# Performance work log

Measured on AMD Instinct MI355X. Metric: run time of the kernel, lower is better.

## Reference

```python
import jax, jax.numpy as jnp
import numpy as np

G = 4096        # graphs
NPG = 32        # nodes per graph
N = G * NPG     # total nodes
D = 256         # hidden (inv node feat) dim
SH = 256        # shared / node-MLP hidden dim
HDG = 50        # graph head dim
HDN = 3         # node head dim
NB = 2          # num branches (dataset IDs)


def setup_inputs() -> dict:
    key = jax.random.key(0)
    ks = jax.random.split(key, 8)
    s = 0.02
    return {
        "x": jax.random.normal(ks[0], (N, D), jnp.float32),
        "dataset_name": jax.random.randint(ks[1], (G,), 0, NB, jnp.int32),
        "batch": (jnp.arange(N) // NPG).astype(jnp.int32),
        "Wgs": jax.random.normal(ks[2], (NB, D, SH), jnp.float32) * s,
        "bgs": jnp.zeros((NB, SH), jnp.float32),
        "Wgh": jax.random.normal(ks[3], (NB, SH, 2 * HDG), jnp.float32) * s,
        "bgh": jnp.zeros((NB, 2 * HDG), jnp.float32),
        "Wn1": jax.random.normal(ks[4], (NB, D, SH), jnp.float32) * s,
        "bn1": jnp.zeros((NB, SH), jnp.float32),
        "Wn2": jax.random.normal(ks[5], (NB, SH, 2 * HDN), jnp.float32) * s,
        "bn2": jnp.zeros((NB, 2 * HDN), jnp.float32),
    }


def reference(x, dataset_name, batch, Wgs, bgs, Wgh, bgh, Wn1, bn1, Wn2, bn2):
    n_nodes = x.shape[0]
    n_graphs = dataset_name.shape[0]

    # ---- graph pooling (mean) : scatter-reduce nodes -> graphs ----
    counts = jax.ops.segment_sum(jnp.ones((n_nodes,), x.dtype), batch, num_segments=n_graphs)
    x_graph = jax.ops.segment_sum(x, batch, num_segments=n_graphs) / counts[:, None]  # [G, D]

    # ---- graph head: per-branch shared MLP + head, then branch dispatch ----
    hg = jax.nn.relu(jnp.einsum("gd,bds->bgs", x_graph, Wgs) + bgs[:, None, :])       # [B, G, SH]
    og = jnp.einsum("bgs,bsh->bgh", hg, Wgh) + bgh[:, None, :]                        # [B, G, 2*HDG]
    out_g = og[dataset_name, jnp.arange(n_graphs)]                                    # [G, 2*HDG]
    g_head = out_g[:, :HDG]
    g_var = out_g[:, HDG:] ** 2

    # ---- node head (mlp type): per-branch MLP on nodes, dispatch by node's graph ID ----
    node_branch = dataset_name[batch]                                                 # [N]
    hn = jax.nn.relu(jnp.einsum("nd,bds->bns", x, Wn1) + bn1[:, None, :])             # [B, N, SH]
    on = jnp.einsum("bns,bsh->bnh", hn, Wn2) + bn2[:, None, :]                        # [B, N, 2*HDN]
    out_n = on[node_branch, jnp.arange(n_nodes)]                                      # [N, 2*HDN]
    n_head = out_n[:, :HDN]
    n_var = out_n[:, HDN:] ** 2

    # (outputs, outputs_var) flattened: heads then variance heads
    return (g_head, n_head, g_var, n_var)
```

## Files before the change

### kernel.cpp

```cpp
#include <hip/hip_runtime.h>
#include <hip/hip_bf16.h>


#define G_   4096
#define NPG_ 32
#define NN_  (G_*NPG_)
#define D_   256
#define SH_  256
#define HDG_ 50
#define HDN_ 3

#define OFF_GH 0
#define OFF_NH (G_*HDG_)
#define OFF_GV (OFF_NH + NN_*HDN_)
#define OFF_NV (OFF_GV + G_*HDG_)

typedef short v8s __attribute__((ext_vector_type(8)));
typedef short v4s __attribute__((ext_vector_type(4)));
typedef float v4f __attribute__((ext_vector_type(4)));

__device__ __forceinline__ float bfu2f(unsigned short u) {
    return __uint_as_float(((unsigned int)u) << 16);
}
__device__ __forceinline__ unsigned short f2bfu(float v) {
    __hip_bfloat16 b = __float2bfloat16(v);
    return *reinterpret_cast<unsigned short*>(&b);
}

#define MFMA16(a, b, c) __builtin_amdgcn_mfma_f32_16x16x32_bf16((a), (b), (c), 0, 0, 0)

__global__ __launch_bounds__(256) void prep(const float* __restrict__ Wn1,
                                            const float* __restrict__ Wgs,
                                            const float* __restrict__ Wgh,
                                            const float* __restrict__ Wn2,
                                            unsigned short* __restrict__ wout,
                                            const int* __restrict__ dsname,
                                            int* __restrict__ glist,
                                            int* __restrict__ gcnt) {
    const int blk = blockIdx.x;
    const int t = threadIdx.x;
    if (blk < 1312) {
        const int idx = blk * 256 + t;
        float v;
        if (idx < 131072) {
            const int b = idx >> 16, rem = idx & 65535, s = rem >> 8, d = rem & 255;
            v = Wn1[b * 65536 + d * 256 + s];
        } else if (idx < 262144) {
            const int i2 = idx - 131072;
            const int np = i2 >> 8, d = i2 & 255;
            v = Wgs[(np >> 8) * 65536 + d * 256 + (np & 255)];
        } else if (idx < 327680) {
            const int i3 = idx - 262144;
            const int npp = i3 >> 8, k = i3 & 255;
            const int b = npp >> 7, c = npp & 127;
            v = (c < 100) ? Wgh[b * 25600 + k * 100 + c] : 0.f;
        } else {
            const int i4 = idx - 327680;
            const int b = i4 >> 12, rem = i4 & 4095, n = rem >> 8, k = rem & 255;
            v = (n < 6) ? Wn2[b * 1536 + k * 6 + n] : 0.f;
        }
        wout[idx] = f2bfu(v);
    } else {
        __shared__ int cnt[2];
        if (t < 2) cnt[t] = 0;
        __syncthreads();
        for (int i = 0; i < 16; i++) {
            const int g = i * 256 + t;
            const int b = dsname[g];
            const int slot = atomicAdd(&cnt[b], 1);
            glist[b * G_ + slot] = g;
        }
        __syncthreads();
        if (t < 2) gcnt[t] = cnt[t];
    }
}

__global__ __launch_bounds__(512) void node_pers2(const float* __restrict__ x,
                                                  const int* __restrict__ glist,
                                                  const int* __restrict__ gcnt,
                                                  const unsigned short* __restrict__ Wn1T,
                                                  const float* __restrict__ bn1,
                                                  const unsigned short* __restrict__ Wn2b,
                                                  const float* __restrict__ bn2,
                                                  unsigned short* __restrict__ xg,
                                                  float* __restrict__ out) {
    __shared__ __align__(16) unsigned short xs[64 * 264];
    __shared__ __align__(16) unsigned short hs[64 * 264];
    __shared__ __align__(16) float red[16 * 256];
    const int t = threadIdx.x;
    const int wave = t >> 6, lane = t & 63;
    const int l15 = lane & 15, quad = lane >> 4;
    const int br = blockIdx.x & 1;
    const int bslot = blockIdx.x >> 1;
    const int cnt = gcnt[br];
    const int ntile = (cnt + 1) >> 1;

    const int base_n = (wave & 1) * 128 + (wave >> 1) * 32;

    v8s B1[2][8];
    float bias1[2];
    #pragma unroll
    for (int nt = 0; nt < 2; nt++) {
        const unsigned short* bp = Wn1T + br * 65536 + (base_n + nt * 16 + l15) * 256 + quad * 8;
        #pragma unroll
        for (int kt = 0; kt < 8; kt++) B1[nt][kt] = *(const v8s*)(bp + kt * 32);
        bias1[nt] = bn1[br * 256 + base_n + nt * 16 + l15];
    }

    v8s B2[8];
    {
        const unsigned short* bp = Wn2b + br * 4096 + l15 * 256 + quad * 8;
        #pragma unroll
        for (int kt = 0; kt < 8; kt++) B2[kt] = *(const v8s*)(bp + kt * 32);
    }
    float bias2 = 0.f;
    if (l15 < 6) bias2 = bn2[br * 6 + l15];

    const int r0 = t >> 6;
    const int colb = (t & 63) * 4;

    float4 pv[8];
    int ga = 0, gb = 0;
    if (bslot < ntile) {
        const int i0 = 2 * bslot, i1 = i0 + 1;
        ga = glist[br * G_ + i0];
        gb = glist[br * G_ + ((i1 < cnt) ? i1 : cnt - 1)];
        const float* xa = x + (size_t)ga * 8192 + r0 * 256 + colb;
        const float* xb = x + (size_t)gb * 8192 + r0 * 256 + colb;
        #pragma unroll
        for (int k = 0; k < 4; k++) {
            pv[k]     = *(const float4*)(xa + k * 2048);
            pv[4 + k] = *(const float4*)(xb + k * 2048);
        }
    }

    for (int ti = bslot; ti < ntile; ti += 128) {
        const int gA = ga, gB = gb;

        float4 sa = make_float4(0.f, 0.f, 0.f, 0.f);
        float4 sb = make_float4(0.f, 0.f, 0.f, 0.f);
        #pragma unroll
        for (int k = 0; k < 4; k++) {
            const float4 va = pv[k], vb = pv[4 + k];
            sa.x += va.x; sa.y += va.y; sa.z += va.z; sa.w += va.w;
            sb.x += vb.x; sb.y += vb.y; sb.z += vb.z; sb.w += vb.w;
            v4s bva, bvb;
            bva[0] = (short)f2bfu(va.x); bva[1] = (short)f2bfu(va.y);
            bva[2] = (short)f2bfu(va.z); bva[3] = (short)f2bfu(va.w);
            bvb[0] = (short)f2bfu(vb.x); bvb[1] = (short)f2bfu(vb.y);
            bvb[2] = (short)f2bfu(vb.z); bvb[3] = (short)f2bfu(vb.w);
            *(v4s*)(&xs[(r0 + 8 * k) * 264 + colb])      = bva;
            *(v4s*)(&xs[(32 + r0 + 8 * k) * 264 + colb]) = bvb;
        }
        *(float4*)(&red[r0 * 256 + colb])       = sa;
        *(float4*)(&red[(8 + r0) * 256 + colb]) = sb;

        {
            const int tn = ti + 128;
            if (tn < ntile) {
                const int i0 = 2 * tn, i1 = i0 + 1;
                ga = glist[br * G_ + i0];
                gb = glist[br * G_ + ((i1 < cnt) ? i1 : cnt - 1)];
                const float* xa = x + (size_t)ga * 8192 + r0 * 256 + colb;
                const float* xb = x + (size_t)gb * 8192 + r0 * 256 + colb;
                #pragma unroll
                for (int k = 0; k < 4; k++) {
                    pv[k]     = *(const float4*)(xa + k * 2048);
                    pv[4 + k] = *(const float4*)(xb + k * 2048);
                }
            }
        }
        __syncthreads();

        {
            const int g = t >> 8, c = t & 255;
            float m = 0.f;
            #pragma unroll
            for (int r = 0; r < 8; r++) m += red[(g * 8 + r) * 256 + c];
            xg[(size_t)(g ? gB : gA) * 256 + c] = f2bfu(m * (1.0f / NPG_));
        }

        v4f acc[4][2];
        #pragma unroll
        for (int mt = 0; mt < 4; mt++)
            #pragma unroll
            for (int nt = 0; nt < 2; nt++) acc[mt][nt] = (v4f){0.f, 0.f, 0.f, 0.f};
        #pragma unroll
        for (int kt = 0; kt < 8; kt++) {
            const int ko = kt * 32 + quad * 8;
            v8s a0 = *(const v8s*)(&xs[(     l15) * 264 + ko]);
            v8s a1 = *(const v8s*)(&xs[(16 + l15) * 264 + ko]);
            v8s a2 = *(const v8s*)(&xs[(32 + l15) * 264 + ko]);
            v8s a3 = *(const v8s*)(&xs[(48 + l15) * 264 + ko]);
            #pragma unroll
            for (int nt = 0; nt < 2; nt++) {
                acc[0][nt] = MFMA16(a0, B1[nt][kt], acc[0][nt]);
                acc[1][nt] = MFMA16(a1, B1[nt][kt], acc[1][nt]);
                acc[2][nt] = MFMA16(a2, B1[nt][kt], acc[2][nt]);
                acc[3][nt] = MFMA16(a3, B1[nt][kt], acc[3][nt]);
            }
        }

        #pragma unroll
        for (int nt = 0; nt < 2; nt++) {
            const int col = base_n + nt * 16 + l15;
            #pragma unroll
            for (int mt = 0; mt < 4; mt++)
                #pragma unroll
                for (int r = 0; r < 4; r++) {
                    const int row = mt * 16 + quad * 4 + r;
                    const float v = acc[mt][nt][r] + bias1[nt];
                    hs[row * 264 + col] = f2bfu(v > 0.f ? v : 0.f);
                }
        }
        __syncthreads();

        if (wave < 4) {
            v4f a2 = (v4f){0.f, 0.f, 0.f, 0.f};
            #pragma unroll
            for (int kt = 0; kt < 8; kt++) {
                v8s av = *(const v8s*)(&hs[(wave * 16 + l15) * 264 + kt * 32 + quad * 8]);
                a2 = MFMA16(av, B2[kt], a2);
            }
            if (l15 < 6) {
                #pragma unroll
                for (int r = 0; r < 4; r++) {
                    const int row = wave * 16 + quad * 4 + r;
                    const int g = (row < 32) ? gA : gB;
                    const int n = g * NPG_ + (row & 31);
                    const float v = a2[r] + bias2;
                    if (l15 < HDN_) out[OFF_NH + n * HDN_ + l15] = v;
                    else            out[OFF_NV + n * HDN_ + (l15 - HDN_)] = v * v;
                }
            }
        }
    }
}

__global__ __launch_bounds__(256) void graph_mfma2(const unsigned short* __restrict__ xg,
                                                   const int* __restrict__ dsname,
                                                   const unsigned short* __restrict__ WgsT,
                                                   const float* __restrict__ bgs,
                                                   const unsigned short* __restrict__ WghP,
                                                   const float* __restrict__ bgh,
                                                   float* __restrict__ out) {
    __shared__ __align__(16) unsigned short xs[32 * 264];
    __shared__ int bls[32];
    const int gbase = blockIdx.x * 32;
    const int t = threadIdx.x;
    const int wave = t >> 6, lane = t & 63;
    const int l15 = lane & 15, quad = lane >> 4;
    if (t < 32) bls[t] = dsname[gbase + t];

    #pragma unroll
    for (int k = 0; k < 4; k++) {
        const int flat = k * 2048 + t * 8;
        *(v8s*)(&xs[(flat >> 8) * 264 + (flat & 255)]) =
            *(const v8s*)(xg + (size_t)gbase * 256 + flat);
    }
    __syncthreads();

    v4f acc[2][8];
    #pragma unroll
    for (int mt = 0; mt < 2; mt++)
        #pragma unroll
        for (int nt = 0; nt < 8; nt++) acc[mt][nt] = (v4f){0.f, 0.f, 0.f, 0.f};

    const unsigned short* Ab = &xs[l15 * 264 + quad * 8];
    const unsigned short* Bb = WgsT + (wave * 128 + l15) * 256 + quad * 8;

    #pragma unroll
    for (int kt = 0; kt < 8; kt++) {
        const int ko = kt * 32;
        v8s a0 = *(const v8s*)(Ab + ko);
        v8s a1 = *(const v8s*)(Ab + 16 * 264 + ko);
        #pragma unroll
        for (int nt = 0; nt < 8; nt++) {
            v8s bv = *(const v8s*)(Bb + nt * 16 * 256 + ko);
            acc[0][nt] = MFMA16(a0, bv, acc[0][nt]);
            acc[1][nt] = MFMA16(a1, bv, acc[1][nt]);
        }
    }
    __syncthreads();

    {
        const int bw = wave >> 1;
        #pragma unroll
        for (int nt = 0; nt < 8; nt++) {
            const int sp = wave * 128 + nt * 16 + l15;
            const int s_local = sp & 255;
            const float bias = bgs[sp];
            #pragma unroll
            for (int mt = 0; mt < 2; mt++)
                #pragma unroll
                for (int r = 0; r < 4; r++) {
                    const int row = mt * 16 + quad * 4 + r;
                    if (bls[row] == bw) {
                        const float v = acc[mt][nt][r] + bias;
                        xs[row * 264 + s_local] = f2bfu(v > 0.f ? v : 0.f);
                    }
                }
        }
    }
    __syncthreads();

    v4f acc2[2][4];
    #pragma unroll
    for (int mt = 0; mt < 2; mt++)
        #pragma unroll
        for (int nt = 0; nt < 4; nt++) acc2[mt][nt] = (v4f){0.f, 0.f, 0.f, 0.f};

    const unsigned short* B2 = WghP + ((wave * 4) * 16 + l15) * 256 + quad * 8;
    #pragma unroll
    for (int kt = 0; kt < 8; kt++) {
        const int ko = kt * 32;
        v8s a0 = *(const v8s*)(&xs[l15 * 264 + ko + quad * 8]);
        v8s a1 = *(const v8s*)(&xs[(16 + l15) * 264 + ko + quad * 8]);
        #pragma unroll
        for (int nt = 0; nt < 4; nt++) {
            v8s bv = *(const v8s*)(B2 + nt * 16 * 256 + ko);
            acc2[0][nt] = MFMA16(a0, bv, acc2[0][nt]);
            acc2[1][nt] = MFMA16(a1, bv, acc2[1][nt]);
        }
    }

    #pragma unroll
    for (int nt = 0; nt < 4; nt++) {
        const int npp  = (wave * 4 + nt) * 16 + l15;
        const int bo   = npp >> 7, c = npp & 127;
        if (c < 2 * HDG_) {
            const float bias = bgh[bo * 2 * HDG_ + c];
            #pragma unroll
            for (int mt = 0; mt < 2; mt++)
                #pragma unroll
                for (int r = 0; r < 4; r++) {
                    const int row = mt * 16 + quad * 4 + r;
                    if (bls[row] == bo) {
                        const float o = acc2[mt][nt][r] + bias;
                        const int g = gbase + row;
                        if (c < HDG_) out[OFF_GH + g * HDG_ + c] = o;
                        else          out[OFF_GV + g * HDG_ + (c - HDG_)] = o * o;
                    }
                }
        }
    }
}

extern "C" void kernel_launch(void* const* d_in, const int* in_sizes, int n_in,
                              void* d_out, int out_size, void* d_ws, size_t ws_size,
                              hipStream_t stream) {
    const float* x      = (const float*)d_in[0];
    const int*   dsname = (const int*)d_in[1];
    const float* Wgs = (const float*)d_in[3];
    const float* bgs = (const float*)d_in[4];
    const float* Wgh = (const float*)d_in[5];
    const float* bgh = (const float*)d_in[6];
    const float* Wn1 = (const float*)d_in[7];
    const float* bn1 = (const float*)d_in[8];
    const float* Wn2 = (const float*)d_in[9];
    const float* bn2 = (const float*)d_in[10];
    float* out = (float*)d_out;

    unsigned short* wsbuf = (unsigned short*)d_ws;
    unsigned short* Wn1T  = wsbuf;
    unsigned short* WgsT  = wsbuf + 131072;
    unsigned short* WghP  = wsbuf + 262144;
    unsigned short* Wn2b  = wsbuf + 327680;
    unsigned short* xg    = wsbuf + 335872;
    int* glist = (int*)((char*)d_ws + 2768896);
    int* gcnt  = (int*)((char*)d_ws + 2801664);

    prep       <<<1313,    256, 0, stream>>>(Wn1, Wgs, Wgh, Wn2, wsbuf, dsname, glist, gcnt);
    node_pers2 <<<256,     512, 0, stream>>>(x, glist, gcnt, Wn1T, bn1, Wn2b, bn2, xg, out);
    graph_mfma2<<<G_ / 32, 256, 0, stream>>>(xg, dsname, WgsT, bgs, WghP, bgh, out);
}
```

Before: 246.8 us.

## Fold weight prep and graph bucketing into the persistent node kernel

Removes the separate prep kernel. Each node block now converts its slice of the graph-head weights to bf16, computes its own per-branch graph list through a block-wide prefix scan over dataset IDs, and loads the Wn1/Wn2 fragments straight from fp32 with a transpose and bf16 conversion done in registers. This drops one kernel launch and the global round trip for glist and the transposed node weights. In exchange every block rescans all dataset IDs and does strided, uncoalesced fp32 weight gathers.

```diff
diff --git a/kernel.cpp b/kernel.cpp
--- a/kernel.cpp
+++ b/kernel.cpp
@@ -19,9 +19,6 @@
 typedef short v4s __attribute__((ext_vector_type(4)));
 typedef float v4f __attribute__((ext_vector_type(4)));
 
-__device__ __forceinline__ float bfu2f(unsigned short u) {
-    return __uint_as_float(((unsigned int)u) << 16);
-}
 __device__ __forceinline__ unsigned short f2bfu(float v) {
     __hip_bfloat16 b = __float2bfloat16(v);
     return *reinterpret_cast<unsigned short*>(&b);
@@ -29,89 +26,115 @@
 
 #define MFMA16(a, b, c) __builtin_amdgcn_mfma_f32_16x16x32_bf16((a), (b), (c), 0, 0, 0)
 
-__global__ __launch_bounds__(256) void prep(const float* __restrict__ Wn1,
-                                            const float* __restrict__ Wgs,
-                                            const float* __restrict__ Wgh,
-                                            const float* __restrict__ Wn2,
-                                            unsigned short* __restrict__ wout,
-                                            const int* __restrict__ dsname,
-                                            int* __restrict__ glist,
-                                            int* __restrict__ gcnt) {
-    const int blk = blockIdx.x;
-    const int t = threadIdx.x;
-    if (blk < 1312) {
-        const int idx = blk * 256 + t;
-        float v;
-        if (idx < 131072) {
-            const int b = idx >> 16, rem = idx & 65535, s = rem >> 8, d = rem & 255;
-            v = Wn1[b * 65536 + d * 256 + s];
-        } else if (idx < 262144) {
-            const int i2 = idx - 131072;
-            const int np = i2 >> 8, d = i2 & 255;
-            v = Wgs[(np >> 8) * 65536 + d * 256 + (np & 255)];
-        } else if (idx < 327680) {
-            const int i3 = idx - 262144;
-            const int npp = i3 >> 8, k = i3 & 255;
-            const int b = npp >> 7, c = npp & 127;
-            v = (c < 100) ? Wgh[b * 25600 + k * 100 + c] : 0.f;
-        } else {
-            const int i4 = idx - 327680;
-            const int b = i4 >> 12, rem = i4 & 4095, n = rem >> 8, k = rem & 255;
-            v = (n < 6) ? Wn2[b * 1536 + k * 6 + n] : 0.f;
-        }
-        wout[idx] = f2bfu(v);
-    } else {
-        __shared__ int cnt[2];
-        if (t < 2) cnt[t] = 0;
-        __syncthreads();
-        for (int i = 0; i < 16; i++) {
-            const int g = i * 256 + t;
-            const int b = dsname[g];
-            const int slot = atomicAdd(&cnt[b], 1);
-            glist[b * G_ + slot] = g;
-        }
-        __syncthreads();
-        if (t < 2) gcnt[t] = cnt[t];
-    }
-}
-
-__global__ __launch_bounds__(512) void node_pers2(const float* __restrict__ x,
-                                                  const int* __restrict__ glist,
-                                                  const int* __restrict__ gcnt,
-                                                  const unsigned short* __restrict__ Wn1T,
-                                                  const float* __restrict__ bn1,
-                                                  const unsigned short* __restrict__ Wn2b,
-                                                  const float* __restrict__ bn2,
-                                                  unsigned short* __restrict__ xg,
-                                                  float* __restrict__ out) {
+__global__ __launch_bounds__(512) void node_all(const float* __restrict__ x,
+                                                const int* __restrict__ dsname,
+                                                const float* __restrict__ Wn1,
+                                                const float* __restrict__ bn1,
+                                                const float* __restrict__ Wn2,
+                                                const float* __restrict__ bn2,
+                                                const float* __restrict__ Wgs,
+                                                const float* __restrict__ Wgh,
+                                                unsigned short* __restrict__ WgsT,
+                                                unsigned short* __restrict__ WghP,
+                                                unsigned short* __restrict__ xg,
+                                                float* __restrict__ out) {
     __shared__ __align__(16) unsigned short xs[64 * 264];
     __shared__ __align__(16) unsigned short hs[64 * 264];
     __shared__ __align__(16) float red[16 * 256];
+    __shared__ int glds[32];
+    __shared__ int scanS[10];
     const int t = threadIdx.x;
     const int wave = t >> 6, lane = t & 63;
     const int l15 = lane & 15, quad = lane >> 4;
     const int br = blockIdx.x & 1;
     const int bslot = blockIdx.x >> 1;
-    const int cnt = gcnt[br];
+
+    {
+        const int e0 = blockIdx.x * 768;
+        #pragma unroll
+        for (int i = 0; i < 2; i++) {
+            const int ii = t + i * 512;
+            if (ii < 768) {
+                const int e = e0 + ii;
+                if (e < 131072) {
+                    const int np = e >> 8, d = e & 255;
+                    WgsT[e] = f2bfu(Wgs[(np >> 8) * 65536 + d * 256 + (np & 255)]);
+                } else {
+                    const int i3 = e - 131072;
+                    const int npp = i3 >> 8, k = i3 & 255;
+                    const int b = npp >> 7, c = npp & 127;
+                    WghP[i3] = f2bfu((c < 100) ? Wgh[b * 25600 + k * 100 + c] : 0.f);
+                }
+            }
+        }
+    }
+
+    int pre, c0;
+    {
+        c0 = 0;
+        #pragma unroll
+        for (int k = 0; k < 8; k++) c0 += (dsname[t * 8 + k] == br) ? 1 : 0;
+        pre = c0;
+        #pragma unroll
+        for (int d = 1; d < 64; d <<= 1) {
+            const int o = __shfl_up(pre, d);
+            if (lane >= d) pre += o;
+        }
+        if (lane == 63) scanS[wave] = pre;
+    }
+    __syncthreads();
+    if (t == 0) {
+        int s = 0;
+        #pragma unroll
+        for (int w = 0; w < 8; w++) { const int v = scanS[w]; scanS[w] = s; s += v; }
+        scanS[8] = s;
+    }
+    __syncthreads();
+    const int cnt = scanS[8];
     const int ntile = (cnt + 1) >> 1;
+    {
+        int slot = scanS[wave] + (pre - c0);
+        for (int k = 0; k < 8; k++) {
+            const int g = t * 8 + k;
+            if (dsname[g] == br) {
+                const int ti2 = slot >> 1;
+                const int q = ti2 - bslot;
+                if (q >= 0 && (q & 127) == 0 && (q >> 7) < 16)
+                    glds[(q >> 7) * 2 + (slot & 1)] = g;
+                if (slot == cnt - 1) scanS[9] = g;
+                slot++;
+            }
+        }
+    }
+    __syncthreads();
 
     const int base_n = (wave & 1) * 128 + (wave >> 1) * 32;
-
     v8s B1[2][8];
     float bias1[2];
     #pragma unroll
     for (int nt = 0; nt < 2; nt++) {
-        const unsigned short* bp = Wn1T + br * 65536 + (base_n + nt * 16 + l15) * 256 + quad * 8;
-        #pragma unroll
-        for (int kt = 0; kt < 8; kt++) B1[nt][kt] = *(const v8s*)(bp + kt * 32);
-        bias1[nt] = bn1[br * 256 + base_n + nt * 16 + l15];
-    }
-
+        const int s = base_n + nt * 16 + l15;
+        const float* wp = Wn1 + br * 65536 + s;
+        #pragma unroll
+        for (int kt = 0; kt < 8; kt++) {
+            v8s f;
+            #pragma unroll
+            for (int j = 0; j < 8; j++)
+                f[j] = (short)f2bfu(wp[(kt * 32 + quad * 8 + j) * 256]);
+            B1[nt][kt] = f;
+        }
+        bias1[nt] = bn1[br * 256 + s];
+    }
     v8s B2[8];
-    {
-        const unsigned short* bp = Wn2b + br * 4096 + l15 * 256 + quad * 8;
-        #pragma unroll
-        for (int kt = 0; kt < 8; kt++) B2[kt] = *(const v8s*)(bp + kt * 32);
+    #pragma unroll
+    for (int kt = 0; kt < 8; kt++) {
+        v8s f;
+        #pragma unroll
+        for (int j = 0; j < 8; j++) {
+            const int k = kt * 32 + quad * 8 + j;
+            f[j] = (l15 < 6) ? (short)f2bfu(Wn2[br * 1536 + k * 6 + l15]) : (short)0;
+        }
+        B2[kt] = f;
     }
     float bias2 = 0.f;
     if (l15 < 6) bias2 = bn2[br * 6 + l15];
@@ -122,9 +145,8 @@
     float4 pv[8];
     int ga = 0, gb = 0;
     if (bslot < ntile) {
-        const int i0 = 2 * bslot, i1 = i0 + 1;
-        ga = glist[br * G_ + i0];
-        gb = glist[br * G_ + ((i1 < cnt) ? i1 : cnt - 1)];
+        ga = glds[0];
+        gb = (2 * bslot + 1 < cnt) ? glds[1] : scanS[9];
         const float* xa = x + (size_t)ga * 8192 + r0 * 256 + colb;
         const float* xb = x + (size_t)gb * 8192 + r0 * 256 + colb;
         #pragma unroll
@@ -158,9 +180,9 @@
         {
             const int tn = ti + 128;
             if (tn < ntile) {
-                const int i0 = 2 * tn, i1 = i0 + 1;
-                ga = glist[br * G_ + i0];
-                gb = glist[br * G_ + ((i1 < cnt) ? i1 : cnt - 1)];
+                const int ix = (tn - bslot) >> 7;
+                ga = glds[ix * 2];
+                gb = (2 * tn + 1 < cnt) ? glds[ix * 2 + 1] : scanS[9];
                 const float* xa = x + (size_t)ga * 8192 + r0 * 256 + colb;
                 const float* xb = x + (size_t)gb * 8192 + r0 * 256 + colb;
                 #pragma unroll
@@ -362,15 +384,11 @@
     float* out = (float*)d_out;
 
     unsigned short* wsbuf = (unsigned short*)d_ws;
-    unsigned short* Wn1T  = wsbuf;
     unsigned short* WgsT  = wsbuf + 131072;
     unsigned short* WghP  = wsbuf + 262144;
-    unsigned short* Wn2b  = wsbuf + 327680;
     unsigned short* xg    = wsbuf + 335872;
-    int* glist = (int*)((char*)d_ws + 2768896);
-    int* gcnt  = (int*)((char*)d_ws + 2801664);
-
-    prep       <<<1313,    256, 0, stream>>>(Wn1, Wgs, Wgh, Wn2, wsbuf, dsname, glist, gcnt);
-    node_pers2 <<<256,     512, 0, stream>>>(x, glist, gcnt, Wn1T, bn1, Wn2b, bn2, xg, out);
+
+    node_all   <<<256,     512, 0, stream>>>(x, dsname, Wn1, bn1, Wn2, bn2,
+                                             Wgs, Wgh, WgsT, WghP, xg, out);
     graph_mfma2<<<G_ / 32, 256, 0, stream>>>(xg, dsname, WgsT, bgs, WghP, bgh, out);
 }
```

Result: no change. 248.9 us (+0.9%).

## Replace persistent node kernel with one-tile-per-block launch and shared LDS buffer

Applied to the files above, without the earlier changes.

The persistent 256-block node kernel, which looped over graph-pair tiles with register prefetch of the next tile, becomes a 4096-block grid where each block handles one graph pair and returns early if it has no work. The hidden-activation LDS buffer is removed and the x tile buffer is reused for it, with an extra barrier added before the overwrite. The smaller LDS footprint is meant to allow more resident blocks per CU, so the hardware scheduler hides load latency in place of the manual prefetch. In exchange, every block reloads the Wn1/Wn2 weight fragments into registers, and about half of the blocks launch only to exit immediately.

```diff
diff --git a/kernel.cpp b/kernel.cpp
--- a/kernel.cpp
+++ b/kernel.cpp
@@ -19,9 +19,6 @@
 typedef short v4s __attribute__((ext_vector_type(4)));
 typedef float v4f __attribute__((ext_vector_type(4)));
 
-__device__ __forceinline__ float bfu2f(unsigned short u) {
-    return __uint_as_float(((unsigned int)u) << 16);
-}
 __device__ __forceinline__ unsigned short f2bfu(float v) {
     __hip_bfloat16 b = __float2bfloat16(v);
     return *reinterpret_cast<unsigned short*>(&b);
@@ -75,25 +72,29 @@
     }
 }
 
-__global__ __launch_bounds__(512) void node_pers2(const float* __restrict__ x,
-                                                  const int* __restrict__ glist,
-                                                  const int* __restrict__ gcnt,
-                                                  const unsigned short* __restrict__ Wn1T,
-                                                  const float* __restrict__ bn1,
-                                                  const unsigned short* __restrict__ Wn2b,
-                                                  const float* __restrict__ bn2,
-                                                  unsigned short* __restrict__ xg,
-                                                  float* __restrict__ out) {
+__global__ __launch_bounds__(512) void node_tile(const float* __restrict__ x,
+                                                 const int* __restrict__ glist,
+                                                 const int* __restrict__ gcnt,
+                                                 const unsigned short* __restrict__ Wn1T,
+                                                 const float* __restrict__ bn1,
+                                                 const unsigned short* __restrict__ Wn2b,
+                                                 const float* __restrict__ bn2,
+                                                 unsigned short* __restrict__ xg,
+                                                 float* __restrict__ out) {
     __shared__ __align__(16) unsigned short xs[64 * 264];
-    __shared__ __align__(16) unsigned short hs[64 * 264];
     __shared__ __align__(16) float red[16 * 256];
     const int t = threadIdx.x;
     const int wave = t >> 6, lane = t & 63;
     const int l15 = lane & 15, quad = lane >> 4;
     const int br = blockIdx.x & 1;
     const int bslot = blockIdx.x >> 1;
+
     const int cnt = gcnt[br];
-    const int ntile = (cnt + 1) >> 1;
+    if (2 * bslot >= cnt) return;
+
+    const int gA = glist[br * G_ + 2 * bslot];
+    const int gB = (2 * bslot + 1 < cnt) ? glist[br * G_ + 2 * bslot + 1]
+                                         : glist[br * G_ + cnt - 1];
 
     const int base_n = (wave & 1) * 128 + (wave >> 1) * 32;
 
@@ -106,42 +107,26 @@
         for (int kt = 0; kt < 8; kt++) B1[nt][kt] = *(const v8s*)(bp + kt * 32);
         bias1[nt] = bn1[br * 256 + base_n + nt * 16 + l15];
     }
-
     v8s B2[8];
     {
         const unsigned short* bp = Wn2b + br * 4096 + l15 * 256 + quad * 8;
         #pragma unroll
         for (int kt = 0; kt < 8; kt++) B2[kt] = *(const v8s*)(bp + kt * 32);
     }
-    float bias2 = 0.f;
-    if (l15 < 6) bias2 = bn2[br * 6 + l15];
+    const float bias2 = (l15 < 6) ? bn2[br * 6 + l15] : 0.f;
 
     const int r0 = t >> 6;
     const int colb = (t & 63) * 4;
 
-    float4 pv[8];
-    int ga = 0, gb = 0;
-    if (bslot < ntile) {
-        const int i0 = 2 * bslot, i1 = i0 + 1;
-        ga = glist[br * G_ + i0];
-        gb = glist[br * G_ + ((i1 < cnt) ? i1 : cnt - 1)];
-        const float* xa = x + (size_t)ga * 8192 + r0 * 256 + colb;
-        const float* xb = x + (size_t)gb * 8192 + r0 * 256 + colb;
-        #pragma unroll
-        for (int k = 0; k < 4; k++) {
-            pv[k]     = *(const float4*)(xa + k * 2048);
-            pv[4 + k] = *(const float4*)(xb + k * 2048);
-        }
-    }
-
-    for (int ti = bslot; ti < ntile; ti += 128) {
-        const int gA = ga, gB = gb;
-
+    {
+        const float* xa = x + (size_t)gA * 8192 + r0 * 256 + colb;
+        const float* xb = x + (size_t)gB * 8192 + r0 * 256 + colb;
         float4 sa = make_float4(0.f, 0.f, 0.f, 0.f);
         float4 sb = make_float4(0.f, 0.f, 0.f, 0.f);
         #pragma unroll
         for (int k = 0; k < 4; k++) {
-            const float4 va = pv[k], vb = pv[4 + k];
+            const float4 va = *(const float4*)(xa + k * 2048);
+            const float4 vb = *(const float4*)(xb + k * 2048);
             sa.x += va.x; sa.y += va.y; sa.z += va.z; sa.w += va.w;
             sb.x += vb.x; sb.y += vb.y; sb.z += vb.z; sb.w += vb.w;
             v4s bva, bvb;
@@ -154,84 +139,69 @@
         }
         *(float4*)(&red[r0 * 256 + colb])       = sa;
         *(float4*)(&red[(8 + r0) * 256 + colb]) = sb;
-
-        {
-            const int tn = ti + 128;
-            if (tn < ntile) {
-                const int i0 = 2 * tn, i1 = i0 + 1;
-                ga = glist[br * G_ + i0];
-                gb = glist[br * G_ + ((i1 < cnt) ? i1 : cnt - 1)];
-                const float* xa = x + (size_t)ga * 8192 + r0 * 256 + colb;
-                const float* xb = x + (size_t)gb * 8192 + r0 * 256 + colb;
-                #pragma unroll
-                for (int k = 0; k < 4; k++) {
-                    pv[k]     = *(const float4*)(xa + k * 2048);
-                    pv[4 + k] = *(const float4*)(xb + k * 2048);
-                }
-            }
-        }
-        __syncthreads();
-
-        {
-            const int g = t >> 8, c = t & 255;
-            float m = 0.f;
-            #pragma unroll
-            for (int r = 0; r < 8; r++) m += red[(g * 8 + r) * 256 + c];
-            xg[(size_t)(g ? gB : gA) * 256 + c] = f2bfu(m * (1.0f / NPG_));
-        }
-
-        v4f acc[4][2];
+    }
+    __syncthreads();
+
+    {
+        const int g = t >> 8, c = t & 255;
+        float m = 0.f;
+        #pragma unroll
+        for (int r = 0; r < 8; r++) m += red[(g * 8 + r) * 256 + c];
+        xg[(size_t)(g ? gB : gA) * 256 + c] = f2bfu(m * (1.0f / NPG_));
+    }
+
+    v4f acc[4][2];
+    #pragma unroll
+    for (int mt = 0; mt < 4; mt++)
+        #pragma unroll
+        for (int nt = 0; nt < 2; nt++) acc[mt][nt] = (v4f){0.f, 0.f, 0.f, 0.f};
+    #pragma unroll
+    for (int kt = 0; kt < 8; kt++) {
+        const int ko = kt * 32 + quad * 8;
+        v8s a0 = *(const v8s*)(&xs[(     l15) * 264 + ko]);
+        v8s a1 = *(const v8s*)(&xs[(16 + l15) * 264 + ko]);
+        v8s a2 = *(const v8s*)(&xs[(32 + l15) * 264 + ko]);
+        v8s a3 = *(const v8s*)(&xs[(48 + l15) * 264 + ko]);
+        #pragma unroll
+        for (int nt = 0; nt < 2; nt++) {
+            acc[0][nt] = MFMA16(a0, B1[nt][kt], acc[0][nt]);
+            acc[1][nt] = MFMA16(a1, B1[nt][kt], acc[1][nt]);
+            acc[2][nt] = MFMA16(a2, B1[nt][kt], acc[2][nt]);
+            acc[3][nt] = MFMA16(a3, B1[nt][kt], acc[3][nt]);
+        }
+    }
+    __syncthreads();
+
+    #pragma unroll
+    for (int nt = 0; nt < 2; nt++) {
+        const int col = base_n + nt * 16 + l15;
         #pragma unroll
         for (int mt = 0; mt < 4; mt++)
             #pragma unroll
-            for (int nt = 0; nt < 2; nt++) acc[mt][nt] = (v4f){0.f, 0.f, 0.f, 0.f};
+            for (int r = 0; r < 4; r++) {
+                const int row = mt * 16 + quad * 4 + r;
+                const float v = acc[mt][nt][r] + bias1[nt];
+                xs[row * 264 + col] = f2bfu(v > 0.f ? v : 0.f);
+            }
+    }
+    __syncthreads();
+
+    if (wave < 4) {
+        v4f a2 = (v4f){0.f, 0.f, 0.f, 0.f};
         #pragma unroll
         for (int kt = 0; kt < 8; kt++) {
-            const int ko = kt * 32 + quad * 8;
-            v8s a0 = *(const v8s*)(&xs[(     l15) * 264 + ko]);
-            v8s a1 = *(const v8s*)(&xs[(16 + l15) * 264 + ko]);
-            v8s a2 = *(const v8s*)(&xs[(32 + l15) * 264 + ko]);
-            v8s a3 = *(const v8s*)(&xs[(48 + l15) * 264 + ko]);
+            v8s av = *(const v8s*)(&xs[(wave * 16 + l15) * 264 + kt * 32 + quad * 8]);
+            a2 = MFMA16(av, B2[kt], a2);
+        }
+        if (l15 < 6) {
             #pragma unroll
-            for (int nt = 0; nt < 2; nt++) {
-                acc[0][nt] = MFMA16(a0, B1[nt][kt], acc[0][nt]);
-                acc[1][nt] = MFMA16(a1, B1[nt][kt], acc[1][nt]);
-                acc[2][nt] = MFMA16(a2, B1[nt][kt], acc[2][nt]);
-                acc[3][nt] = MFMA16(a3, B1[nt][kt], acc[3][nt]);
-            }
-        }
-
-        #pragma unroll
-        for (int nt = 0; nt < 2; nt++) {
-            const int col = base_n + nt * 16 + l15;
-            #pragma unroll
-            for (int mt = 0; mt < 4; mt++)
-                #pragma unroll
-                for (int r = 0; r < 4; r++) {
-                    const int row = mt * 16 + quad * 4 + r;
-                    const float v = acc[mt][nt][r] + bias1[nt];
-                    hs[row * 264 + col] = f2bfu(v > 0.f ? v : 0.f);
-                }
-        }
-        __syncthreads();
-
-        if (wave < 4) {
-            v4f a2 = (v4f){0.f, 0.f, 0.f, 0.f};
-            #pragma unroll
-            for (int kt = 0; kt < 8; kt++) {
-                v8s av = *(const v8s*)(&hs[(wave * 16 + l15) * 264 + kt * 32 + quad * 8]);
-                a2 = MFMA16(av, B2[kt], a2);
-            }
-            if (l15 < 6) {
-                #pragma unroll
-                for (int r = 0; r < 4; r++) {
-                    const int row = wave * 16 + quad * 4 + r;
-                    const int g = (row < 32) ? gA : gB;
-                    const int n = g * NPG_ + (row & 31);
-                    const float v = a2[r] + bias2;
-                    if (l15 < HDN_) out[OFF_NH + n * HDN_ + l15] = v;
-                    else            out[OFF_NV + n * HDN_ + (l15 - HDN_)] = v * v;
-                }
+            for (int r = 0; r < 4; r++) {
+                const int row = wave * 16 + quad * 4 + r;
+                const int g = (row < 32) ? gA : gB;
+                const int n = g * NPG_ + (row & 31);
+                const float v = a2[r] + bias2;
+                if (l15 < HDN_) out[OFF_NH + n * HDN_ + l15] = v;
+                else            out[OFF_NV + n * HDN_ + (l15 - HDN_)] = v * v;
             }
         }
     }
@@ -370,7 +340,7 @@
     int* glist = (int*)((char*)d_ws + 2768896);
     int* gcnt  = (int*)((char*)d_ws + 2801664);
 
-    prep       <<<1313,    256, 0, stream>>>(Wn1, Wgs, Wgh, Wn2, wsbuf, dsname, glist, gcnt);
-    node_pers2 <<<256,     512, 0, stream>>>(x, glist, gcnt, Wn1T, bn1, Wn2b, bn2, xg, out);
-    graph_mfma2<<<G_ / 32, 256, 0, stream>>>(xg, dsname, WgsT, bgs, WghP, bgh, out);
-}
+    prep       <<<1313, 256, 0, stream>>>(Wn1, Wgs, Wgh, Wn2, wsbuf, dsname, glist, gcnt);
+    node_tile  <<<4096, 512, 0, stream>>>(x, glist, gcnt, Wn1T, bn1, Wn2b, bn2, xg, out);
+    graph_mfma2<<<G_/32, 256, 0, stream>>>(xg, dsname, WgsT, bgs, WghP, bgh, out);
+}
```

Result: slower. 282.2 us (+14.3%).
